# Performance work log

Hardware: AMD Instinct MI355X
Metric: run time of the kernel (lower is better)

## Reference

```python
import jax, jax.numpy as jnp
import numpy as np

H, DK = 8, 64
INNER = H * DK  # 512


def rel_shift(x):
    # Transformer-XL relative shift (NeMo style): pad left, reshape, drop first row.
    b, h, q, p = x.shape
    x = jnp.pad(x, ((0, 0), (0, 0), (0, 0), (1, 0)))
    x = x.reshape(b, h, p + 1, q)[:, :, 1:]
    return x.reshape(b, h, q, p)


def setup_inputs() -> dict:
    key = jax.random.key(0)
    ks = jax.random.split(key, 16)
    B, T, D = 8, 1024, 512
    s_d = 1.0 / np.sqrt(D)
    s_i = 1.0 / np.sqrt(INNER)
    return {
        "x": jax.random.normal(ks[0], (B, T, D), jnp.float32),
        "pos_emb": jax.random.normal(ks[1], (1, 2 * T - 1, INNER), jnp.float32),
        "w_qkv": jax.random.normal(ks[2], (D, 3 * INNER), jnp.float32) * s_d,
        "w_q": jax.random.normal(ks[3], (INNER, INNER), jnp.float32) * s_i,
        "b_q": jnp.zeros((INNER,), jnp.float32),
        "w_k": jax.random.normal(ks[4], (INNER, INNER), jnp.float32) * s_i,
        "b_k": jnp.zeros((INNER,), jnp.float32),
        "w_v": jax.random.normal(ks[5], (INNER, INNER), jnp.float32) * s_i,
        "b_v": jnp.zeros((INNER,), jnp.float32),
        "w_pos": jax.random.normal(ks[6], (INNER, INNER), jnp.float32) * s_i,
        "bias_u": jax.random.normal(ks[7], (H, DK), jnp.float32) * 0.02,
        "bias_v": jax.random.normal(ks[8], (H, DK), jnp.float32) * 0.02,
        "w_ao": jax.random.normal(ks[9], (INNER, INNER), jnp.float32) * s_i,
        "b_ao": jnp.zeros((INNER,), jnp.float32),
        "w_o": jax.random.normal(ks[10], (INNER, D), jnp.float32) * s_i,
        "b_o": jnp.zeros((D,), jnp.float32),
    }


def reference(x, pos_emb, w_qkv, w_q, b_q, w_k, b_k, w_v, b_v, w_pos,
              bias_u, bias_v, w_ao, b_ao, w_o, b_o):
    B, T, D = x.shape
    # wrapper qkv projection (no bias), then chunk
    q, k, v = jnp.split(x @ w_qkv, 3, axis=-1)
    # RelPositionMultiHeadAttention internal projections
    q = (q @ w_q + b_q).reshape(B, T, H, DK)                       # (b,t,h,d)
    k = (k @ w_k + b_k).reshape(B, T, H, DK).transpose(0, 2, 1, 3)  # (b,h,t,d)
    v = (v @ w_v + b_v).reshape(B, T, H, DK).transpose(0, 2, 1, 3)  # (b,h,t,d)
    p = (pos_emb @ w_pos).reshape(pos_emb.shape[0], -1, H, DK).transpose(0, 2, 1, 3)  # (1,h,2t-1,d)
    q_u = (q + bias_u).transpose(0, 2, 1, 3)  # (b,h,t,d)
    q_v = (q + bias_v).transpose(0, 2, 1, 3)
    matrix_ac = jnp.einsum('bhqd,bhkd->bhqk', q_u, k)      # (b,h,t,t)
    matrix_bd = jnp.einsum('bhqd,xhpd->bhqp', q_v, p)      # (b,h,t,2t-1)
    matrix_bd = rel_shift(matrix_bd)[..., :T]
    scores = (matrix_ac + matrix_bd) * (1.0 / np.sqrt(DK))
    attn = jax.nn.softmax(scores, axis=-1)  # mask=None, dropout inactive at eval
    out = jnp.einsum('bhqk,bhkd->bhqd', attn, v)
    out = out.transpose(0, 2, 1, 3).reshape(B, T, INNER)
    out = out @ w_ao + b_ao   # attention linear_out
    return out @ w_o + b_o    # wrapper to_out
```

## Files before the change

### kernel.cpp

```cpp
#include <hip/hip_runtime.h>
#include <hip/hip_bf16.h>
#include <math.h>

#define H_     8
#define DK_    64
#define INNER_ 512
#define B_     8
#define T_     1024
#define D_     512
#define PLEN_  2047
#define BT_    8192

typedef __attribute__((ext_vector_type(8))) short bf16x8;
typedef __attribute__((ext_vector_type(4))) float f32x4;
typedef __attribute__((ext_vector_type(4))) unsigned short u16x4;
typedef __attribute__((ext_vector_type(8))) unsigned short u16x8;

__device__ __forceinline__ unsigned short f2bf(float f) {
    unsigned u = __float_as_uint(f);
    u += 0x7fffu + ((u >> 16) & 1u);
    return (unsigned short)(u >> 16);
}
__device__ __forceinline__ float bf2f(unsigned short s) {
    return __uint_as_float(((unsigned)s) << 16);
}
__device__ __forceinline__ f32x4 mfma16(bf16x8 a, bf16x8 b, f32x4 c) {
    return __builtin_amdgcn_mfma_f32_16x16x32_bf16(a, b, c, 0, 0, 0);
}
__device__ __forceinline__ void gload16(const unsigned short* g, unsigned short* l) {
    __builtin_amdgcn_global_load_lds(
        (const __attribute__((address_space(1))) void*)g,
        (__attribute__((address_space(3))) void*)l,
        16, 0, 0);
}
#define BARRIER()  __builtin_amdgcn_s_barrier()
#define SCHEDBAR() __builtin_amdgcn_sched_barrier(0)
#define VMCNT(N)   asm volatile("s_waitcnt vmcnt(" #N ")" ::: "memory")

#define QSCALE 0.125f

struct SplitA {
    const float* s[4];
    unsigned short* h[4];
    unsigned short* l[4];
    long n[4];
};
__global__ __launch_bounds__(256) void split4(SplitA a)
{
    const int seg = blockIdx.y;
    long i4 = ((long)blockIdx.x * 256 + threadIdx.x) * 4;
    if (i4 >= a.n[seg]) return;
    f32x4 v = *(const f32x4*)(a.s[seg] + i4);
    u16x4 hh, ll;
    #pragma unroll
    for (int i = 0; i < 4; ++i) {
        unsigned short hb = f2bf(v[i]);
        hh[i] = hb;
        ll[i] = f2bf(v[i] - bf2f(hb));
    }
    *(u16x4*)(a.h[seg] + i4) = hh;
    *(u16x4*)(a.l[seg] + i4) = ll;
}

struct PrepW {
    const float* w[5];
    unsigned short* wh[5];
    unsigned short* wl[5];
};
__global__ __launch_bounds__(256) void prep_wb(PrepW p)
{
    const int z = blockIdx.z;
    const float* w = p.w[z];
    unsigned short* wh = p.wh[z];
    unsigned short* wl = p.wl[z];
    __shared__ float sW[32][36];
    const int t = threadIdx.x;
    const int n0 = blockIdx.x * 32, k0 = blockIdx.y * 32;
    {
        int kr = t >> 3, c4 = (t & 7) * 4;
        f32x4 v = *(const f32x4*)(w + (size_t)(k0 + kr) * 512 + n0 + c4);
        #pragma unroll
        for (int i = 0; i < 4; ++i) sW[kr][c4 + i] = v[i];
    }
    __syncthreads();
    {
        int nr = t >> 3, kc = (t & 7) * 4;
        u16x4 hv, lv;
        #pragma unroll
        for (int i = 0; i < 4; ++i) {
            float f = sW[kc + i][nr];
            unsigned short hb = f2bf(f);
            hv[i] = hb;
            lv[i] = f2bf(f - bf2f(hb));
        }
        *(u16x4*)(wh + (size_t)(n0 + nr) * 512 + k0 + kc) = hv;
        *(u16x4*)(wl + (size_t)(n0 + nr) * 512 + k0 + kc) = lv;
    }
}

__global__ __launch_bounds__(256) void misc_k(
    const float* __restrict__ b_ao, const float* __restrict__ w_o,
    const float* __restrict__ b_o, float* __restrict__ be,
    unsigned short* __restrict__ pb_base)
{
    if (blockIdx.x < 2) {
        int n = blockIdx.x * 256 + threadIdx.x;
        float s = b_o[n];
        for (int j = 0; j < 512; ++j) s += b_ao[j] * w_o[(size_t)j * 512 + n];
        be[n] = s;
    } else {
        ((unsigned int*)pb_base)[threadIdx.x] = 0u;
    }
}

template<int MF, bool ALO>
__device__ __forceinline__ void gemm_core(
    f32x4 (&acc)[MF][4],
    const unsigned short* __restrict__ Ah_g,
    const unsigned short* __restrict__ Al_g, int lda,
    const unsigned short* __restrict__ Wh_g,
    const unsigned short* __restrict__ Wl_g,
    int M, int row0, int col0,
    unsigned short* sAh, unsigned short* sAl,
    unsigned short* sWh, unsigned short* sWl)
{
    const int t = threadIdx.x;
    const int lane = t & 63, w = t >> 6;
    const int wm = w >> 1, wn = w & 1;
    const int ln15 = lane & 15, g4 = lane >> 4;
    const int ASZ = MF * 32 * 32;
    const int WSZ = 128 * 32;
    constexpr int NLD = (MF / 2) * (ALO ? 2 : 1) + 4;

    auto stage = [&](int kt, int buf) {
        #pragma unroll
        for (int l = 0; l < MF / 2; ++l) {
            int e = l * 256 + w * 64 + lane;
            int row = e >> 2, slot = e & 3;
            int ss = slot ^ (row & 3);
            int gr = row0 + row;
            if (gr > M - 1) gr = M - 1;
            size_t ga = (size_t)gr * lda + kt * 32 + ss * 8;
            gload16(Ah_g + ga, sAh + buf * ASZ + (l * 256 + w * 64) * 8);
            if constexpr (ALO)
                gload16(Al_g + ga, sAl + buf * ASZ + (l * 256 + w * 64) * 8);
        }
        #pragma unroll
        for (int l = 0; l < 2; ++l) {
            int e = l * 256 + w * 64 + lane;
            int row = e >> 2, slot = e & 3;
            int ss = slot ^ (row & 3);
            size_t gw = (size_t)(col0 + row) * 512 + kt * 32 + ss * 8;
            gload16(Wh_g + gw, sWh + buf * WSZ + (l * 256 + w * 64) * 8);
            gload16(Wl_g + gw, sWl + buf * WSZ + (l * 256 + w * 64) * 8);
        }
    };
    auto comp = [&](int buf) {
        bf16x8 fah[MF], fal[MF], fwh[4], fwl[4];
        #pragma unroll
        for (int i = 0; i < MF; ++i) {
            int ar = wm * (MF * 16) + i * 16 + ln15;
            int sa = (g4 ^ (ar & 3)) * 8;
            fah[i] = *(const bf16x8*)&sAh[buf * ASZ + ar * 32 + sa];
            if constexpr (ALO)
                fal[i] = *(const bf16x8*)&sAl[buf * ASZ + ar * 32 + sa];
        }
        #pragma unroll
        for (int j = 0; j < 4; ++j) {
            int wr = wn * 64 + j * 16 + ln15;
            int sw = (g4 ^ (wr & 3)) * 8;
            fwh[j] = *(const bf16x8*)&sWh[buf * WSZ + wr * 32 + sw];
            fwl[j] = *(const bf16x8*)&sWl[buf * WSZ + wr * 32 + sw];
        }
        __builtin_amdgcn_s_setprio(1);
        #pragma unroll
        for (int mi = 0; mi < MF; ++mi)
            #pragma unroll
            for (int ni = 0; ni < 4; ++ni) {
                acc[mi][ni] = mfma16(fah[mi], fwh[ni], acc[mi][ni]);
                acc[mi][ni] = mfma16(fah[mi], fwl[ni], acc[mi][ni]);
                if constexpr (ALO)
                    acc[mi][ni] = mfma16(fal[mi], fwh[ni], acc[mi][ni]);
            }
        __builtin_amdgcn_s_setprio(0);
    };

    stage(0, 0);
    for (int k2 = 0; k2 < 8; ++k2) {
        BARRIER();
        stage(2 * k2 + 1, 1);
        if constexpr (NLD == 6) { VMCNT(6); } else { VMCNT(8); }
        BARRIER(); SCHEDBAR();
        comp(0);
        BARRIER();
        if (k2 < 7) {
            stage(2 * k2 + 2, 0);
            if constexpr (NLD == 6) { VMCNT(6); } else { VMCNT(8); }
        } else {
            VMCNT(0);
        }
        BARRIER(); SCHEDBAR();
        comp(1);
    }
}

#define GEMM_LDS3(MF) \
    __shared__ __align__(16) unsigned short sAh[2][MF * 32 * 32]; \
    __shared__ __align__(16) unsigned short sAl[2][MF * 32 * 32]; \
    __shared__ __align__(16) unsigned short sWh[2][128 * 32];     \
    __shared__ __align__(16) unsigned short sWl[2][128 * 32];
#define GEMM_LDS2(MF) \
    __shared__ __align__(16) unsigned short sAh[2][MF * 32 * 32]; \
    __shared__ __align__(16) unsigned short sWh[2][128 * 32];     \
    __shared__ __align__(16) unsigned short sWl[2][128 * 32];

__global__ __launch_bounds__(256, 3) void gemm_qkv(
    const unsigned short* __restrict__ Ah_g,
    const unsigned short* __restrict__ Wh_g,
    const unsigned short* __restrict__ Wl_g,
    const float* __restrict__ b_q, const float* __restrict__ bu,
    const float* __restrict__ bv, const float* __restrict__ b_k,
    const float* __restrict__ b_v,
    unsigned short* __restrict__ qu, unsigned short* __restrict__ qv,
    unsigned short* __restrict__ kb, unsigned short* __restrict__ vt)
{
    GEMM_LDS2(4)
    f32x4 acc[4][4];
    #pragma unroll
    for (int i = 0; i < 4; ++i)
        #pragma unroll
        for (int j = 0; j < 4; ++j) acc[i][j] = (f32x4){0.f, 0.f, 0.f, 0.f};
    const int row0 = blockIdx.y * 128, col0 = blockIdx.x * 128;
    gemm_core<4, false>(acc, Ah_g, nullptr, 512, Wh_g, Wl_g, BT_, row0, col0,
                        &sAh[0][0], &sAh[0][0], &sWh[0][0], &sWl[0][0]);

    const int t = threadIdx.x;
    const int lane = t & 63, w = t >> 6;
    const int wm = w >> 1, wn = w & 1;
    const int ln15 = lane & 15, g4 = lane >> 4;
    const int grp = col0 >> 9;

    if (grp == 2) {
        #pragma unroll
        for (int mi = 0; mi < 4; ++mi) {
            int gr0 = row0 + wm * 64 + mi * 16 + g4 * 4;
            int bb = gr0 >> 10, t0 = gr0 & 1023;
            #pragma unroll
            for (int ni = 0; ni < 4; ++ni) {
                int gcl = (col0 & 511) + wn * 64 + ni * 16 + ln15;
                float bias = b_v[gcl];
                u16x4 vv;
                #pragma unroll
                for (int r4 = 0; r4 < 4; ++r4) vv[r4] = f2bf(acc[mi][ni][r4] + bias);
                *(u16x4*)(vt + ((size_t)(bb * 512 + gcl)) * 1024 + t0) = vv;
            }
        }
    } else {
        #pragma unroll
        for (int mi = 0; mi < 4; ++mi)
            #pragma unroll
            for (int r4 = 0; r4 < 4; ++r4) {
                int gr = row0 + wm * 64 + mi * 16 + g4 * 4 + r4;
                #pragma unroll
                for (int ni = 0; ni < 4; ++ni) {
                    int gcl = (col0 & 511) + wn * 64 + ni * 16 + ln15;
                    float a = acc[mi][ni][r4];
                    if (grp == 0) {
                        float base = a + b_q[gcl];
                        qu[(size_t)gr * 512 + gcl] = f2bf((base + bu[gcl]) * QSCALE);
                        qv[(size_t)gr * 512 + gcl] = f2bf((base + bv[gcl]) * QSCALE);
                    } else {
                        kb[(size_t)gr * 512 + gcl] = f2bf(a + b_k[gcl]);
                    }
                }
            }
    }
}

__global__ __launch_bounds__(256, 3) void gemm_pos(
    const unsigned short* __restrict__ Ah_g,
    const unsigned short* __restrict__ Wh_g,
    const unsigned short* __restrict__ Wl_g,
    unsigned short* __restrict__ pb0)
{
    GEMM_LDS2(4)
    f32x4 acc[4][4];
    #pragma unroll
    for (int i = 0; i < 4; ++i)
        #pragma unroll
        for (int j = 0; j < 4; ++j) acc[i][j] = (f32x4){0.f, 0.f, 0.f, 0.f};
    const int row0 = blockIdx.y * 128, col0 = blockIdx.x * 128;
    gemm_core<4, false>(acc, Ah_g, nullptr, 512, Wh_g, Wl_g, PLEN_, row0, col0,
                        &sAh[0][0], &sAh[0][0], &sWh[0][0], &sWl[0][0]);

    const int t = threadIdx.x;
    const int lane = t & 63, w = t >> 6;
    const int wm = w >> 1, wn = w & 1;
    const int ln15 = lane & 15, g4 = lane >> 4;
    #pragma unroll
    for (int mi = 0; mi < 4; ++mi)
        #pragma unroll
        for (int r4 = 0; r4 < 4; ++r4) {
            int gr = row0 + wm * 64 + mi * 16 + g4 * 4 + r4;
            if (gr >= PLEN_) continue;
            #pragma unroll
            for (int ni = 0; ni < 4; ++ni) {
                int gc = col0 + wn * 64 + ni * 16 + ln15;
                pb0[(size_t)gr * 512 + gc] = f2bf(acc[mi][ni][r4]);
            }
        }
}

struct WeffA {
    const unsigned short* ah[4];
    const unsigned short* al[4];
    int lda[4];
    const unsigned short* wh[4];
    const unsigned short* wl[4];
    float* c[4];
};
__global__ __launch_bounds__(256, 3) void gemm_weff(WeffA a)
{
    GEMM_LDS3(2)
    const int z = blockIdx.z;
    f32x4 acc[2][4];
    #pragma unroll
    for (int i = 0; i < 2; ++i)
        #pragma unroll
        for (int j = 0; j < 4; ++j) acc[i][j] = (f32x4){0.f, 0.f, 0.f, 0.f};
    const int row0 = blockIdx.y * 64, col0 = blockIdx.x * 128;
    gemm_core<2, true>(acc, a.ah[z], a.al[z], a.lda[z], a.wh[z], a.wl[z],
                       512, row0, col0,
                       &sAh[0][0], &sAl[0][0], &sWh[0][0], &sWl[0][0]);

    const int t = threadIdx.x;
    const int lane = t & 63, w = t >> 6;
    const int wm = w >> 1, wn = w & 1;
    const int ln15 = lane & 15, g4 = lane >> 4;
    float* C = a.c[z];
    #pragma unroll
    for (int mi = 0; mi < 2; ++mi)
        #pragma unroll
        for (int r4 = 0; r4 < 4; ++r4) {
            int gr = row0 + wm * 32 + mi * 16 + g4 * 4 + r4;
            #pragma unroll
            for (int ni = 0; ni < 4; ++ni) {
                int gc = col0 + wn * 64 + ni * 16 + ln15;
                C[(size_t)gr * 512 + gc] = acc[mi][ni][r4];
            }
        }
}

__global__ __launch_bounds__(256, 3) void gemm_out(
    const unsigned short* __restrict__ Ah_g,
    const unsigned short* __restrict__ Al_g,
    const unsigned short* __restrict__ Wh_g,
    const unsigned short* __restrict__ Wl_g,
    const float* __restrict__ beff, float* __restrict__ C)
{
    GEMM_LDS3(2)
    f32x4 acc[2][4];
    #pragma unroll
    for (int i = 0; i < 2; ++i)
        #pragma unroll
        for (int j = 0; j < 4; ++j) acc[i][j] = (f32x4){0.f, 0.f, 0.f, 0.f};
    const int row0 = blockIdx.y * 64, col0 = blockIdx.x * 128;
    gemm_core<2, true>(acc, Ah_g, Al_g, 512, Wh_g, Wl_g, BT_, row0, col0,
                       &sAh[0][0], &sAl[0][0], &sWh[0][0], &sWl[0][0]);

    const int t = threadIdx.x;
    const int lane = t & 63, w = t >> 6;
    const int wm = w >> 1, wn = w & 1;
    const int ln15 = lane & 15, g4 = lane >> 4;
    #pragma unroll
    for (int mi = 0; mi < 2; ++mi)
        #pragma unroll
        for (int r4 = 0; r4 < 4; ++r4) {
            int gr = row0 + wm * 32 + mi * 16 + g4 * 4 + r4;
            #pragma unroll
            for (int ni = 0; ni < 4; ++ni) {
                int gc = col0 + wn * 64 + ni * 16 + ln15;
                C[(size_t)gr * 512 + gc] = acc[mi][ni][r4] + beff[gc];
            }
        }
}

__global__ __launch_bounds__(256, 2) void attn_v9(
    const unsigned short* __restrict__ qu_g,
    const unsigned short* __restrict__ qv_g,
    const unsigned short* __restrict__ kb_g,
    const unsigned short* __restrict__ vt_g,
    const unsigned short* __restrict__ pb_g,
    unsigned short* __restrict__ atth,
    unsigned short* __restrict__ attl)
{
    __shared__ __align__(16) unsigned short sK[2][64 * 64];
    __shared__ __align__(16) unsigned short sP[2][64 * 64];
    __shared__ __align__(16) unsigned short sV[2][64 * 64];
    __shared__ __align__(16) unsigned short ringb[64][132];
    __shared__ __align__(16) unsigned short sProb[64][72];

    const int t = threadIdx.x;
    const int lane = t & 63, w = t >> 6;
    const int ln15 = lane & 15, g4 = lane >> 4;

    const int wg = blockIdx.x;
    const int idx = (wg & 7) * 128 + (wg >> 3);
    const int q0 = (idx & 15) * 64;
    const int bh = idx >> 4;
    const int h = bh & 7, b = bh >> 3;
    const size_t tok0 = (size_t)b * T_;
    const int hd = h * DK_;
    const int qq = w * 16 + ln15;

    auto stage_chunk = [&](int c, int buf) {
        #pragma unroll
        for (int l = 0; l < 2; ++l) {
            int e = l * 256 + w * 64 + lane;
            int row = e >> 3, slot = e & 7;
            int sl = slot ^ (row & 7);
            int lofs = buf * 4096 + (l * 256 + w * 64) * 8;
            gload16(kb_g + (tok0 + c * 64 + row) * INNER_ + hd + sl * 8, &sK[0][lofs]);
            gload16(vt_g + ((size_t)(b * H_ + h) * DK_ + row) * T_ + c * 64 + sl * 8, &sV[0][lofs]);
            long p = (long)(c * 64 - q0 + 1023 + row);
            gload16(pb_g + p * INNER_ + hd + sl * 8, &sP[0][lofs]);
        }
    };

    #pragma unroll
    for (int l = 0; l < 2; ++l) {
        int e = l * 256 + w * 64 + lane;
        int row = e >> 3, slot = e & 7;
        int sl = slot ^ (row & 7);
        size_t src = (tok0 + q0 + row) * INNER_ + hd + sl * 8;
        gload16(qu_g + src, &sK[0][(l * 256 + w * 64) * 8]);
        gload16(qv_g + src, &sP[0][(l * 256 + w * 64) * 8]);
    }
    __syncthreads();
    bf16x8 fqu[2], fqv[2];
    #pragma unroll
    for (int ki = 0; ki < 2; ++ki) {
        int sl = (ki * 4 + g4) ^ (qq & 7);
        fqu[ki] = *(const bf16x8*)&sK[0][qq * 64 + sl * 8];
        fqv[ki] = *(const bf16x8*)&sP[0][qq * 64 + sl * 8];
    }
    __syncthreads();

    #pragma unroll
    for (int l = 0; l < 2; ++l) {
        int e = l * 256 + w * 64 + lane;
        int row = e >> 3, slot = e & 7;
        int sl = slot ^ (row & 7);
        long p = (long)(959 - q0 + row);
        gload16(pb_g + p * INNER_ + hd + sl * 8, &sP[0][4096 + (l * 256 + w * 64) * 8]);
    }
    stage_chunk(0, 0);
    VMCNT(6);
    BARRIER(); SCHEDBAR();

    #pragma unroll
    for (int n = 0; n < 4; ++n) {
        f32x4 bdv = {0.f, 0.f, 0.f, 0.f};
        #pragma unroll
        for (int ki = 0; ki < 2; ++ki) {
            int prow = n * 16 + ln15;
            int sl = (ki * 4 + g4) ^ (prow & 7);
            bf16x8 pf = *(const bf16x8*)&sP[0][4096 + prow * 64 + sl * 8];
            bdv = mfma16(pf, fqv[ki], bdv);
        }
        #pragma unroll
        for (int r4 = 0; r4 < 4; ++r4)
            ringb[qq][(n * 16 + g4 * 4 + r4 + qq) & 127] = f2bf(bdv[r4]);
    }

    float m = -1e30f, den = 0.f;
    f32x4 o[4];
    #pragma unroll
    for (int i = 0; i < 4; ++i) o[i] = (f32x4){0.f, 0.f, 0.f, 0.f};

    auto compute_chunk = [&](int c, int buf) {
        const int bofs = buf * 4096;
        f32x4 sc[4], bd[4];
        #pragma unroll
        for (int n = 0; n < 4; ++n) {
            sc[n] = (f32x4){0.f, 0.f, 0.f, 0.f};
            bd[n] = (f32x4){0.f, 0.f, 0.f, 0.f};
        }
        __builtin_amdgcn_s_setprio(1);
        #pragma unroll
        for (int ki = 0; ki < 2; ++ki)
            #pragma unroll
            for (int n = 0; n < 4; ++n) {
                int krow = n * 16 + ln15;
                int sl = (ki * 4 + g4) ^ (krow & 7);
                bf16x8 kf = *(const bf16x8*)&sK[0][bofs + krow * 64 + sl * 8];
                sc[n] = mfma16(kf, fqu[ki], sc[n]);
                bf16x8 pf = *(const bf16x8*)&sP[0][bofs + krow * 64 + sl * 8];
                bd[n] = mfma16(pf, fqv[ki], bd[n]);
            }
        __builtin_amdgcn_s_setprio(0);

        const int pbase = (c & 1) ? 0 : 64;
        #pragma unroll
        for (int n = 0; n < 4; ++n)
            #pragma unroll
            for (int r4 = 0; r4 < 4; ++r4)
                ringb[qq][(pbase + n * 16 + g4 * 4 + r4 + qq) & 127] = f2bf(bd[n][r4]);

        float s[4][4];
        float mx = -1e30f;
        #pragma unroll
        for (int n = 0; n < 4; ++n) {
            const int st2 = (c * 64 + 64 + n * 16 + g4 * 4) & 127;
            u16x4 rv = *(const u16x4*)&ringb[qq][st2];
            #pragma unroll
            for (int r4 = 0; r4 < 4; ++r4) {
                float v = sc[n][r4] + bf2f(rv[r4]);
                s[n][r4] = v;
                mx = fmaxf(mx, v);
            }
        }
        mx = fmaxf(mx, __shfl_xor(mx, 16));
        mx = fmaxf(mx, __shfl_xor(mx, 32));
        float newm = fmaxf(m, mx);
        float scale = __expf(m - newm);
        m = newm;
        float ls = 0.f;
        #pragma unroll
        for (int n = 0; n < 4; ++n) {
            u16x4 pv4;
            #pragma unroll
            for (int r4 = 0; r4 < 4; ++r4) {
                float p = __expf(s[n][r4] - newm);
                ls += p;
                pv4[r4] = f2bf(p);
            }
            *(u16x4*)&sProb[qq][n * 16 + g4 * 4] = pv4;
        }
        ls += __shfl_xor(ls, 16);
        ls += __shfl_xor(ls, 32);
        den = den * scale + ls;
        #pragma unroll
        for (int n2 = 0; n2 < 4; ++n2) {
            o[n2][0] *= scale; o[n2][1] *= scale;
            o[n2][2] *= scale; o[n2][3] *= scale;
        }

        __builtin_amdgcn_s_setprio(1);
        #pragma unroll
        for (int ki = 0; ki < 2; ++ki) {
            bf16x8 pa = *(const bf16x8*)&sProb[qq][ki * 32 + g4 * 8];
            #pragma unroll
            for (int n2 = 0; n2 < 4; ++n2) {
                int drow = n2 * 16 + ln15;
                int sl = (ki * 4 + g4) ^ (drow & 7);
                bf16x8 vf = *(const bf16x8*)&sV[0][bofs + drow * 64 + sl * 8];
                o[n2] = mfma16(vf, pa, o[n2]);
            }
        }
        __builtin_amdgcn_s_setprio(0);
    };

    for (int c2 = 0; c2 < 8; ++c2) {
        const int c = 2 * c2;
        BARRIER();
        stage_chunk(c + 1, 1);
        VMCNT(6);
        BARRIER(); SCHEDBAR();
        compute_chunk(c, 0);

        BARRIER();
        if (c2 < 7) {
            stage_chunk(c + 2, 0);
            VMCNT(6);
        } else {
            VMCNT(0);
        }
        BARRIER(); SCHEDBAR();
        compute_chunk(c + 1, 1);
    }

    const float inv = 1.0f / den;
    #pragma unroll
    for (int n2 = 0; n2 < 4; ++n2) {
        u16x4 hv, lv;
        #pragma unroll
        for (int r4 = 0; r4 < 4; ++r4) {
            float val = o[n2][r4] * inv;
            unsigned short hb = f2bf(val);
            hv[r4] = hb;
            lv[r4] = f2bf(val - bf2f(hb));
        }
        size_t oidx = (tok0 + q0 + qq) * INNER_ + hd + n2 * 16 + g4 * 4;
        *(u16x4*)(atth + oidx) = hv;
        *(u16x4*)(attl + oidx) = lv;
    }
}

extern "C" void kernel_launch(void* const* d_in, const int* in_sizes, int n_in,
                              void* d_out, int out_size, void* d_ws, size_t ws_size,
                              hipStream_t stream)
{
    const float* x     = (const float*)d_in[0];
    const float* pos   = (const float*)d_in[1];
    const float* w_qkv = (const float*)d_in[2];
    const float* w_q   = (const float*)d_in[3];
    const float* b_q   = (const float*)d_in[4];
    const float* w_k   = (const float*)d_in[5];
    const float* b_k   = (const float*)d_in[6];
    const float* w_v   = (const float*)d_in[7];
    const float* b_v   = (const float*)d_in[8];
    const float* w_pos = (const float*)d_in[9];
    const float* bu    = (const float*)d_in[10];
    const float* bv    = (const float*)d_in[11];
    const float* w_ao  = (const float*)d_in[12];
    const float* b_ao  = (const float*)d_in[13];
    const float* w_o   = (const float*)d_in[14];
    const float* b_o   = (const float*)d_in[15];
    float* out = (float*)d_out;

    unsigned short* u = (unsigned short*)d_ws;
    const size_t SZ = (size_t)BT_ * INNER_;
    unsigned short* xh   = u;
    unsigned short* xl   = xh + SZ;
    unsigned short* qu   = xl + SZ;
    unsigned short* qv   = qu + SZ;
    unsigned short* kb   = qv + SZ;
    unsigned short* vt   = kb + SZ;
    unsigned short* atth = vt + SZ;
    unsigned short* attl = atth + SZ;
    unsigned short* pb_base = attl + SZ;
    unsigned short* pb0  = pb_base + 512;
    unsigned short* posh = pb_base + 1049600;
    unsigned short* posl = posh + 1049600;
    unsigned short* wqkvh = posl + 1049600;
    unsigned short* wqkvl = wqkvh + 786432;
    unsigned short* waoh  = wqkvl + 786432;
    unsigned short* waol  = waoh + 262144;
    unsigned short* w5    = waol + 262144;
    unsigned short* wq_h = w5;              unsigned short* wq_l = w5 + 262144;
    unsigned short* wk_h = w5 + 2*262144;   unsigned short* wk_l = w5 + 3*262144;
    unsigned short* wv_h = w5 + 4*262144;   unsigned short* wv_l = w5 + 5*262144;
    unsigned short* wo_h = w5 + 6*262144;   unsigned short* wo_l = w5 + 7*262144;
    unsigned short* wp_h = w5 + 8*262144;   unsigned short* wp_l = w5 + 9*262144;
    float* weffC = (float*)(w5 + 10*262144);
    unsigned short* wcat_h = (unsigned short*)(weffC + 4*262144);
    unsigned short* wcat_l = wcat_h + 786432;
    unsigned short* woe_h  = wcat_l + 786432;
    unsigned short* woe_l  = woe_h + 262144;
    float* beff = (float*)(woe_l + 262144);

    dim3 blk(256);

    SplitA sa;
    sa.s[0] = x;     sa.h[0] = xh;    sa.l[0] = xl;    sa.n[0] = (long)SZ;
    sa.s[1] = w_qkv; sa.h[1] = wqkvh; sa.l[1] = wqkvl; sa.n[1] = 786432L;
    sa.s[2] = w_ao;  sa.h[2] = waoh;  sa.l[2] = waol;  sa.n[2] = 262144L;
    sa.s[3] = pos;   sa.h[3] = posh;  sa.l[3] = posl;  sa.n[3] = (long)PLEN_ * 512;
    split4<<<dim3(4096, 4), blk, 0, stream>>>(sa);

    PrepW p5;
    p5.w[0] = w_q;   p5.wh[0] = wq_h; p5.wl[0] = wq_l;
    p5.w[1] = w_k;   p5.wh[1] = wk_h; p5.wl[1] = wk_l;
    p5.w[2] = w_v;   p5.wh[2] = wv_h; p5.wl[2] = wv_l;
    p5.w[3] = w_o;   p5.wh[3] = wo_h; p5.wl[3] = wo_l;
    p5.w[4] = w_pos; p5.wh[4] = wp_h; p5.wl[4] = wp_l;
    prep_wb<<<dim3(16, 16, 5), blk, 0, stream>>>(p5);

    WeffA wa;
    wa.ah[0] = wqkvh;        wa.al[0] = wqkvl;        wa.lda[0] = 1536;
    wa.ah[1] = wqkvh + 512;  wa.al[1] = wqkvl + 512;  wa.lda[1] = 1536;
    wa.ah[2] = wqkvh + 1024; wa.al[2] = wqkvl + 1024; wa.lda[2] = 1536;
    wa.ah[3] = waoh;         wa.al[3] = waol;         wa.lda[3] = 512;
    wa.wh[0] = wq_h; wa.wl[0] = wq_l;
    wa.wh[1] = wk_h; wa.wl[1] = wk_l;
    wa.wh[2] = wv_h; wa.wl[2] = wv_l;
    wa.wh[3] = wo_h; wa.wl[3] = wo_l;
    wa.c[0] = weffC;             wa.c[1] = weffC + 262144;
    wa.c[2] = weffC + 2*262144;  wa.c[3] = weffC + 3*262144;
    gemm_weff<<<dim3(4, 8, 4), blk, 0, stream>>>(wa);

    PrepW p4;
    p4.w[0] = weffC;            p4.wh[0] = wcat_h;            p4.wl[0] = wcat_l;
    p4.w[1] = weffC + 262144;   p4.wh[1] = wcat_h + 262144;   p4.wl[1] = wcat_l + 262144;
    p4.w[2] = weffC + 2*262144; p4.wh[2] = wcat_h + 2*262144; p4.wl[2] = wcat_l + 2*262144;
    p4.w[3] = weffC + 3*262144; p4.wh[3] = woe_h;             p4.wl[3] = woe_l;
    p4.w[4] = nullptr; p4.wh[4] = nullptr; p4.wl[4] = nullptr;
    prep_wb<<<dim3(16, 16, 4), blk, 0, stream>>>(p4);

    misc_k<<<3, blk, 0, stream>>>(b_ao, w_o, b_o, beff, pb_base);

    gemm_qkv<<<dim3(12, 64), blk, 0, stream>>>(xh, wcat_h, wcat_l,
        b_q, bu, bv, b_k, b_v, qu, qv, kb, vt);
    gemm_pos<<<dim3(4, 16), blk, 0, stream>>>(posh, wp_h, wp_l, pb0);

    attn_v9<<<1024, blk, 0, stream>>>(qu, qv, kb, vt, pb0, atth, attl);

    gemm_out<<<dim3(4, 128), blk, 0, stream>>>(atth, attl, woe_h, woe_l, beff, out);
}
```

Measured before the change: 195.5 us.

## Halve attention KV chunk size to raise occupancy and skip unused low splits

The attention kernel now processes 32-key chunks instead of 64. This halves the shared-memory staging buffers and probability tile, and lets launch bounds target three workgroups per CU instead of two. The pipeline becomes a simple double buffer over 32 iterations, and the relative-position ring buffer indexing is reworked to match. Separately, the split kernel skips writing low-part bf16 halves for x and pos_emb, which downstream code does not use. The cost is twice as many barriers and loop iterations, and shorter MFMA runs per barrier.

```diff
diff --git a/kernel.cpp b/kernel.cpp
--- a/kernel.cpp
+++ b/kernel.cpp
@@ -44,6 +44,7 @@
     unsigned short* h[4];
     unsigned short* l[4];
     long n[4];
+    int wantl[4];
 };
 __global__ __launch_bounds__(256) void split4(SplitA a)
 {
@@ -59,7 +60,7 @@
         ll[i] = f2bf(v[i] - bf2f(hb));
     }
     *(u16x4*)(a.h[seg] + i4) = hh;
-    *(u16x4*)(a.l[seg] + i4) = ll;
+    if (a.wantl[seg]) *(u16x4*)(a.l[seg] + i4) = ll;
 }
 
 struct PrepW {
@@ -385,7 +386,7 @@
         }
 }
 
-__global__ __launch_bounds__(256, 2) void attn_v9(
+__global__ __launch_bounds__(256, 3) void attn_v10(
     const unsigned short* __restrict__ qu_g,
     const unsigned short* __restrict__ qv_g,
     const unsigned short* __restrict__ kb_g,
@@ -394,11 +395,11 @@
     unsigned short* __restrict__ atth,
     unsigned short* __restrict__ attl)
 {
-    __shared__ __align__(16) unsigned short sK[2][64 * 64];
-    __shared__ __align__(16) unsigned short sP[2][64 * 64];
-    __shared__ __align__(16) unsigned short sV[2][64 * 64];
+    __shared__ __align__(16) unsigned short sK[2][2048];
+    __shared__ __align__(16) unsigned short sP[2][2048];
+    __shared__ __align__(16) unsigned short sV[2][2048];
     __shared__ __align__(16) unsigned short ringb[64][132];
-    __shared__ __align__(16) unsigned short sProb[64][72];
+    __shared__ __align__(16) unsigned short sProb[64][36];
 
     const int t = threadIdx.x;
     const int lane = t & 63, w = t >> 6;
@@ -414,64 +415,79 @@
     const int qq = w * 16 + ln15;
 
     auto stage_chunk = [&](int c, int buf) {
-        #pragma unroll
-        for (int l = 0; l < 2; ++l) {
-            int e = l * 256 + w * 64 + lane;
+        int e = w * 64 + lane;
+        {
             int row = e >> 3, slot = e & 7;
             int sl = slot ^ (row & 7);
-            int lofs = buf * 4096 + (l * 256 + w * 64) * 8;
-            gload16(kb_g + (tok0 + c * 64 + row) * INNER_ + hd + sl * 8, &sK[0][lofs]);
-            gload16(vt_g + ((size_t)(b * H_ + h) * DK_ + row) * T_ + c * 64 + sl * 8, &sV[0][lofs]);
-            long p = (long)(c * 64 - q0 + 1023 + row);
-            gload16(pb_g + p * INNER_ + hd + sl * 8, &sP[0][lofs]);
+            gload16(kb_g + (tok0 + c * 32 + row) * INNER_ + hd + sl * 8,
+                    &sK[buf][w * 512]);
+        }
+        {
+            int row = e >> 2, slot = e & 3;
+            int sl = slot ^ (row & 3);
+            gload16(vt_g + ((size_t)(b * H_ + h) * DK_ + row) * T_ + c * 32 + sl * 8,
+                    &sV[buf][w * 512]);
+        }
+        {
+            int row = e >> 3, slot = e & 7;
+            int sl = slot ^ (row & 7);
+            long p = (long)(c * 32 - q0 + 1023 + row);
+            gload16(pb_g + p * INNER_ + hd + sl * 8, &sP[buf][w * 512]);
         }
     };
 
+    const unsigned short* sKf = &sK[0][0];
+    const unsigned short* sPf = &sP[0][0];
     #pragma unroll
     for (int l = 0; l < 2; ++l) {
-        int e = l * 256 + w * 64 + lane;
+        int e = l * 256 + t;
         int row = e >> 3, slot = e & 7;
         int sl = slot ^ (row & 7);
         size_t src = (tok0 + q0 + row) * INNER_ + hd + sl * 8;
-        gload16(qu_g + src, &sK[0][(l * 256 + w * 64) * 8]);
-        gload16(qv_g + src, &sP[0][(l * 256 + w * 64) * 8]);
+        gload16(qu_g + src, &sK[l][w * 512]);
+        gload16(qv_g + src, &sP[l][w * 512]);
     }
     __syncthreads();
     bf16x8 fqu[2], fqv[2];
     #pragma unroll
     for (int ki = 0; ki < 2; ++ki) {
         int sl = (ki * 4 + g4) ^ (qq & 7);
-        fqu[ki] = *(const bf16x8*)&sK[0][qq * 64 + sl * 8];
-        fqv[ki] = *(const bf16x8*)&sP[0][qq * 64 + sl * 8];
+        fqu[ki] = *(const bf16x8*)&sKf[qq * 64 + sl * 8];
+        fqv[ki] = *(const bf16x8*)&sPf[qq * 64 + sl * 8];
     }
     __syncthreads();
 
     #pragma unroll
     for (int l = 0; l < 2; ++l) {
-        int e = l * 256 + w * 64 + lane;
+        int e = l * 256 + t;
         int row = e >> 3, slot = e & 7;
         int sl = slot ^ (row & 7);
         long p = (long)(959 - q0 + row);
-        gload16(pb_g + p * INNER_ + hd + sl * 8, &sP[0][4096 + (l * 256 + w * 64) * 8]);
-    }
+        gload16(pb_g + p * INNER_ + hd + sl * 8, &sP[l][w * 512]);
+    }
+    VMCNT(0);
+    BARRIER(); SCHEDBAR();
+
+    #pragma unroll
+    for (int hh2 = 0; hh2 < 2; ++hh2)
+        #pragma unroll
+        for (int n = 0; n < 2; ++n) {
+            f32x4 bdv = {0.f, 0.f, 0.f, 0.f};
+            #pragma unroll
+            for (int ki = 0; ki < 2; ++ki) {
+                int prow = hh2 * 32 + n * 16 + ln15;
+                int sl = (ki * 4 + g4) ^ (prow & 7);
+                bf16x8 pf = *(const bf16x8*)&sPf[prow * 64 + sl * 8];
+                bdv = mfma16(pf, fqv[ki], bdv);
+            }
+            #pragma unroll
+            for (int r4 = 0; r4 < 4; ++r4)
+                ringb[qq][(hh2 * 32 + n * 16 + g4 * 4 + r4 + qq + 64) & 127] =
+                    f2bf(bdv[r4]);
+        }
+    BARRIER();
+
     stage_chunk(0, 0);
-    VMCNT(6);
-    BARRIER(); SCHEDBAR();
-
-    #pragma unroll
-    for (int n = 0; n < 4; ++n) {
-        f32x4 bdv = {0.f, 0.f, 0.f, 0.f};
-        #pragma unroll
-        for (int ki = 0; ki < 2; ++ki) {
-            int prow = n * 16 + ln15;
-            int sl = (ki * 4 + g4) ^ (prow & 7);
-            bf16x8 pf = *(const bf16x8*)&sP[0][4096 + prow * 64 + sl * 8];
-            bdv = mfma16(pf, fqv[ki], bdv);
-        }
-        #pragma unroll
-        for (int r4 = 0; r4 < 4; ++r4)
-            ringb[qq][(n * 16 + g4 * 4 + r4 + qq) & 127] = f2bf(bdv[r4]);
-    }
 
     float m = -1e30f, den = 0.f;
     f32x4 o[4];
@@ -479,10 +495,9 @@
     for (int i = 0; i < 4; ++i) o[i] = (f32x4){0.f, 0.f, 0.f, 0.f};
 
     auto compute_chunk = [&](int c, int buf) {
-        const int bofs = buf * 4096;
-        f32x4 sc[4], bd[4];
-        #pragma unroll
-        for (int n = 0; n < 4; ++n) {
+        f32x4 sc[2], bd[2];
+        #pragma unroll
+        for (int n = 0; n < 2; ++n) {
             sc[n] = (f32x4){0.f, 0.f, 0.f, 0.f};
             bd[n] = (f32x4){0.f, 0.f, 0.f, 0.f};
         }
@@ -490,28 +505,28 @@
         #pragma unroll
         for (int ki = 0; ki < 2; ++ki)
             #pragma unroll
-            for (int n = 0; n < 4; ++n) {
+            for (int n = 0; n < 2; ++n) {
                 int krow = n * 16 + ln15;
                 int sl = (ki * 4 + g4) ^ (krow & 7);
-                bf16x8 kf = *(const bf16x8*)&sK[0][bofs + krow * 64 + sl * 8];
+                bf16x8 kf = *(const bf16x8*)&sK[buf][krow * 64 + sl * 8];
                 sc[n] = mfma16(kf, fqu[ki], sc[n]);
-                bf16x8 pf = *(const bf16x8*)&sP[0][bofs + krow * 64 + sl * 8];
+                bf16x8 pf = *(const bf16x8*)&sP[buf][krow * 64 + sl * 8];
                 bd[n] = mfma16(pf, fqv[ki], bd[n]);
             }
         __builtin_amdgcn_s_setprio(0);
 
-        const int pbase = (c & 1) ? 0 : 64;
-        #pragma unroll
-        for (int n = 0; n < 4; ++n)
+        #pragma unroll
+        for (int n = 0; n < 2; ++n)
             #pragma unroll
             for (int r4 = 0; r4 < 4; ++r4)
-                ringb[qq][(pbase + n * 16 + g4 * 4 + r4 + qq) & 127] = f2bf(bd[n][r4]);
-
-        float s[4][4];
+                ringb[qq][(c * 32 + n * 16 + g4 * 4 + r4 + qq) & 127] =
+                    f2bf(bd[n][r4]);
+
+        float s[2][4];
         float mx = -1e30f;
         #pragma unroll
-        for (int n = 0; n < 4; ++n) {
-            const int st2 = (c * 64 + 64 + n * 16 + g4 * 4) & 127;
+        for (int n = 0; n < 2; ++n) {
+            const int st2 = (c * 32 + n * 16 + g4 * 4) & 127;
             u16x4 rv = *(const u16x4*)&ringb[qq][st2];
             #pragma unroll
             for (int r4 = 0; r4 < 4; ++r4) {
@@ -527,7 +542,7 @@
         m = newm;
         float ls = 0.f;
         #pragma unroll
-        for (int n = 0; n < 4; ++n) {
+        for (int n = 0; n < 2; ++n) {
             u16x4 pv4;
             #pragma unroll
             for (int r4 = 0; r4 < 4; ++r4) {
@@ -547,37 +562,27 @@
         }
 
         __builtin_amdgcn_s_setprio(1);
-        #pragma unroll
-        for (int ki = 0; ki < 2; ++ki) {
-            bf16x8 pa = *(const bf16x8*)&sProb[qq][ki * 32 + g4 * 8];
-            #pragma unroll
-            for (int n2 = 0; n2 < 4; ++n2) {
-                int drow = n2 * 16 + ln15;
-                int sl = (ki * 4 + g4) ^ (drow & 7);
-                bf16x8 vf = *(const bf16x8*)&sV[0][bofs + drow * 64 + sl * 8];
-                o[n2] = mfma16(vf, pa, o[n2]);
-            }
+        bf16x8 pa = *(const bf16x8*)&sProb[qq][g4 * 8];
+        #pragma unroll
+        for (int n2 = 0; n2 < 4; ++n2) {
+            int drow = n2 * 16 + ln15;
+            int sl4 = g4 ^ (drow & 3);
+            bf16x8 vf = *(const bf16x8*)&sV[buf][drow * 32 + sl4 * 8];
+            o[n2] = mfma16(vf, pa, o[n2]);
         }
         __builtin_amdgcn_s_setprio(0);
     };
 
-    for (int c2 = 0; c2 < 8; ++c2) {
-        const int c = 2 * c2;
+    for (int c = 0; c < 32; ++c) {
         BARRIER();
-        stage_chunk(c + 1, 1);
-        VMCNT(6);
-        BARRIER(); SCHEDBAR();
-        compute_chunk(c, 0);
-
-        BARRIER();
-        if (c2 < 7) {
-            stage_chunk(c + 2, 0);
-            VMCNT(6);
+        if (c < 31) {
+            stage_chunk(c + 1, (c + 1) & 1);
+            VMCNT(3);
         } else {
             VMCNT(0);
         }
         BARRIER(); SCHEDBAR();
-        compute_chunk(c + 1, 1);
+        compute_chunk(c, c & 1);
     }
 
     const float inv = 1.0f / den;
@@ -653,10 +658,10 @@
     dim3 blk(256);
 
     SplitA sa;
-    sa.s[0] = x;     sa.h[0] = xh;    sa.l[0] = xl;    sa.n[0] = (long)SZ;
-    sa.s[1] = w_qkv; sa.h[1] = wqkvh; sa.l[1] = wqkvl; sa.n[1] = 786432L;
-    sa.s[2] = w_ao;  sa.h[2] = waoh;  sa.l[2] = waol;  sa.n[2] = 262144L;
-    sa.s[3] = pos;   sa.h[3] = posh;  sa.l[3] = posl;  sa.n[3] = (long)PLEN_ * 512;
+    sa.s[0] = x;     sa.h[0] = xh;    sa.l[0] = xl;    sa.n[0] = (long)SZ;          sa.wantl[0] = 0;
+    sa.s[1] = w_qkv; sa.h[1] = wqkvh; sa.l[1] = wqkvl; sa.n[1] = 786432L;           sa.wantl[1] = 1;
+    sa.s[2] = w_ao;  sa.h[2] = waoh;  sa.l[2] = waol;  sa.n[2] = 262144L;           sa.wantl[2] = 1;
+    sa.s[3] = pos;   sa.h[3] = posh;  sa.l[3] = posl;  sa.n[3] = (long)PLEN_ * 512; sa.wantl[3] = 0;
     split4<<<dim3(4096, 4), blk, 0, stream>>>(sa);
 
     PrepW p5;
@@ -694,7 +699,7 @@
         b_q, bu, bv, b_k, b_v, qu, qv, kb, vt);
     gemm_pos<<<dim3(4, 16), blk, 0, stream>>>(posh, wp_h, wp_l, pb0);
 
-    attn_v9<<<1024, blk, 0, stream>>>(qu, qv, kb, vt, pb0, atth, attl);
+    attn_v10<<<1024, blk, 0, stream>>>(qu, qv, kb, vt, pb0, atth, attl);
 
     gemm_out<<<dim3(4, 128), blk, 0, stream>>>(atth, attl, woe_h, woe_l, beff, out);
 }
```

Result: slower. 211.7 us (+8.3%).

## Fuse pos GEMM into QKV GEMM launch, skip unused low splits, simplify attention sync

Applied to the files above, without the earlier changes.

Merges the positional projection GEMM into the QKV GEMM grid as an extra column of blocks, removing one launch and letting the two GEMMs run concurrently. The split kernel no longer writes low-part bf16 halves for x and pos_emb, since those are never read. In the attention kernel, the hand-tuned partial vmcnt waits and raw barriers are replaced with plain __syncthreads, which waits for all outstanding loads each step and may lose the prefetch/compute overlap.

```diff
diff --git a/kernel.cpp b/kernel.cpp
--- a/kernel.cpp
+++ b/kernel.cpp
@@ -44,6 +44,7 @@
     unsigned short* h[4];
     unsigned short* l[4];
     long n[4];
+    int wantl[4];
 };
 __global__ __launch_bounds__(256) void split4(SplitA a)
 {
@@ -59,7 +60,7 @@
         ll[i] = f2bf(v[i] - bf2f(hb));
     }
     *(u16x4*)(a.h[seg] + i4) = hh;
-    *(u16x4*)(a.l[seg] + i4) = ll;
+    if (a.wantl[seg]) *(u16x4*)(a.l[seg] + i4) = ll;
 }
 
 struct PrepW {
@@ -214,15 +215,19 @@
     __shared__ __align__(16) unsigned short sWh[2][128 * 32];     \
     __shared__ __align__(16) unsigned short sWl[2][128 * 32];
 
-__global__ __launch_bounds__(256, 3) void gemm_qkv(
+__global__ __launch_bounds__(256, 3) void gemm_qkvp(
     const unsigned short* __restrict__ Ah_g,
     const unsigned short* __restrict__ Wh_g,
     const unsigned short* __restrict__ Wl_g,
+    const unsigned short* __restrict__ posh,
+    const unsigned short* __restrict__ wp_h,
+    const unsigned short* __restrict__ wp_l,
     const float* __restrict__ b_q, const float* __restrict__ bu,
     const float* __restrict__ bv, const float* __restrict__ b_k,
     const float* __restrict__ b_v,
     unsigned short* __restrict__ qu, unsigned short* __restrict__ qv,
-    unsigned short* __restrict__ kb, unsigned short* __restrict__ vt)
+    unsigned short* __restrict__ kb, unsigned short* __restrict__ vt,
+    unsigned short* __restrict__ pb0)
 {
     GEMM_LDS2(4)
     f32x4 acc[4][4];
@@ -230,16 +235,43 @@
     for (int i = 0; i < 4; ++i)
         #pragma unroll
         for (int j = 0; j < 4; ++j) acc[i][j] = (f32x4){0.f, 0.f, 0.f, 0.f};
-    const int row0 = blockIdx.y * 128, col0 = blockIdx.x * 128;
-    gemm_core<4, false>(acc, Ah_g, nullptr, 512, Wh_g, Wl_g, BT_, row0, col0,
+
+    const int bx = blockIdx.x, by = blockIdx.y;
+    const bool isPos = (bx == 12);
+    int row0, col0, M;
+    const unsigned short *Ag, *Whg, *Wlg;
+    if (isPos) {
+        row0 = (by >> 2) * 128; col0 = (by & 3) * 128;
+        Ag = posh; Whg = wp_h; Wlg = wp_l; M = PLEN_;
+    } else {
+        row0 = by * 128; col0 = bx * 128;
+        Ag = Ah_g; Whg = Wh_g; Wlg = Wl_g; M = BT_;
+    }
+    gemm_core<4, false>(acc, Ag, nullptr, 512, Whg, Wlg, M, row0, col0,
                         &sAh[0][0], &sAh[0][0], &sWh[0][0], &sWl[0][0]);
 
     const int t = threadIdx.x;
     const int lane = t & 63, w = t >> 6;
     const int wm = w >> 1, wn = w & 1;
     const int ln15 = lane & 15, g4 = lane >> 4;
+
+    if (isPos) {
+        #pragma unroll
+        for (int mi = 0; mi < 4; ++mi)
+            #pragma unroll
+            for (int r4 = 0; r4 < 4; ++r4) {
+                int gr = row0 + wm * 64 + mi * 16 + g4 * 4 + r4;
+                if (gr >= PLEN_) continue;
+                #pragma unroll
+                for (int ni = 0; ni < 4; ++ni) {
+                    int gc = col0 + wn * 64 + ni * 16 + ln15;
+                    pb0[(size_t)gr * 512 + gc] = f2bf(acc[mi][ni][r4]);
+                }
+            }
+        return;
+    }
+
     const int grp = col0 >> 9;
-
     if (grp == 2) {
         #pragma unroll
         for (int mi = 0; mi < 4; ++mi) {
@@ -277,40 +309,6 @@
     }
 }
 
-__global__ __launch_bounds__(256, 3) void gemm_pos(
-    const unsigned short* __restrict__ Ah_g,
-    const unsigned short* __restrict__ Wh_g,
-    const unsigned short* __restrict__ Wl_g,
-    unsigned short* __restrict__ pb0)
-{
-    GEMM_LDS2(4)
-    f32x4 acc[4][4];
-    #pragma unroll
-    for (int i = 0; i < 4; ++i)
-        #pragma unroll
-        for (int j = 0; j < 4; ++j) acc[i][j] = (f32x4){0.f, 0.f, 0.f, 0.f};
-    const int row0 = blockIdx.y * 128, col0 = blockIdx.x * 128;
-    gemm_core<4, false>(acc, Ah_g, nullptr, 512, Wh_g, Wl_g, PLEN_, row0, col0,
-                        &sAh[0][0], &sAh[0][0], &sWh[0][0], &sWl[0][0]);
-
-    const int t = threadIdx.x;
-    const int lane = t & 63, w = t >> 6;
-    const int wm = w >> 1, wn = w & 1;
-    const int ln15 = lane & 15, g4 = lane >> 4;
-    #pragma unroll
-    for (int mi = 0; mi < 4; ++mi)
-        #pragma unroll
-        for (int r4 = 0; r4 < 4; ++r4) {
-            int gr = row0 + wm * 64 + mi * 16 + g4 * 4 + r4;
-            if (gr >= PLEN_) continue;
-            #pragma unroll
-            for (int ni = 0; ni < 4; ++ni) {
-                int gc = col0 + wn * 64 + ni * 16 + ln15;
-                pb0[(size_t)gr * 512 + gc] = f2bf(acc[mi][ni][r4]);
-            }
-        }
-}
-
 struct WeffA {
     const unsigned short* ah[4];
     const unsigned short* al[4];
@@ -385,7 +383,7 @@
         }
 }
 
-__global__ __launch_bounds__(256, 2) void attn_v9(
+__global__ __launch_bounds__(256, 2) void attn_v12(
     const unsigned short* __restrict__ qu_g,
     const unsigned short* __restrict__ qv_g,
     const unsigned short* __restrict__ kb_g,
@@ -455,8 +453,7 @@
         gload16(pb_g + p * INNER_ + hd + sl * 8, &sP[0][4096 + (l * 256 + w * 64) * 8]);
     }
     stage_chunk(0, 0);
-    VMCNT(6);
-    BARRIER(); SCHEDBAR();
+    __syncthreads();
 
     #pragma unroll
     for (int n = 0; n < 4; ++n) {
@@ -472,6 +469,7 @@
         for (int r4 = 0; r4 < 4; ++r4)
             ringb[qq][(n * 16 + g4 * 4 + r4 + qq) & 127] = f2bf(bdv[r4]);
     }
+    __syncthreads();
 
     float m = -1e30f, den = 0.f;
     f32x4 o[4];
@@ -562,22 +560,13 @@
     };
 
     for (int c2 = 0; c2 < 8; ++c2) {
-        const int c = 2 * c2;
-        BARRIER();
+        int c = c2 * 2;
         stage_chunk(c + 1, 1);
-        VMCNT(6);
-        BARRIER(); SCHEDBAR();
         compute_chunk(c, 0);
-
-        BARRIER();
-        if (c2 < 7) {
-            stage_chunk(c + 2, 0);
-            VMCNT(6);
-        } else {
-            VMCNT(0);
-        }
-        BARRIER(); SCHEDBAR();
+        __syncthreads();
+        if (c2 < 7) stage_chunk(c + 2, 0);
         compute_chunk(c + 1, 1);
+        __syncthreads();
     }
 
     const float inv = 1.0f / den;
@@ -653,10 +642,10 @@
     dim3 blk(256);
 
     SplitA sa;
-    sa.s[0] = x;     sa.h[0] = xh;    sa.l[0] = xl;    sa.n[0] = (long)SZ;
-    sa.s[1] = w_qkv; sa.h[1] = wqkvh; sa.l[1] = wqkvl; sa.n[1] = 786432L;
-    sa.s[2] = w_ao;  sa.h[2] = waoh;  sa.l[2] = waol;  sa.n[2] = 262144L;
-    sa.s[3] = pos;   sa.h[3] = posh;  sa.l[3] = posl;  sa.n[3] = (long)PLEN_ * 512;
+    sa.s[0] = x;     sa.h[0] = xh;    sa.l[0] = xl;    sa.n[0] = (long)SZ;          sa.wantl[0] = 0;
+    sa.s[1] = w_qkv; sa.h[1] = wqkvh; sa.l[1] = wqkvl; sa.n[1] = 786432L;           sa.wantl[1] = 1;
+    sa.s[2] = w_ao;  sa.h[2] = waoh;  sa.l[2] = waol;  sa.n[2] = 262144L;           sa.wantl[2] = 1;
+    sa.s[3] = pos;   sa.h[3] = posh;  sa.l[3] = posl;  sa.n[3] = (long)PLEN_ * 512; sa.wantl[3] = 0;
     split4<<<dim3(4096, 4), blk, 0, stream>>>(sa);
 
     PrepW p5;
@@ -690,11 +679,11 @@
 
     misc_k<<<3, blk, 0, stream>>>(b_ao, w_o, b_o, beff, pb_base);
 
-    gemm_qkv<<<dim3(12, 64), blk, 0, stream>>>(xh, wcat_h, wcat_l,
-        b_q, bu, bv, b_k, b_v, qu, qv, kb, vt);
-    gemm_pos<<<dim3(4, 16), blk, 0, stream>>>(posh, wp_h, wp_l, pb0);
-
-    attn_v9<<<1024, blk, 0, stream>>>(qu, qv, kb, vt, pb0, atth, attl);
+    gemm_qkvp<<<dim3(13, 64), blk, 0, stream>>>(xh, wcat_h, wcat_l,
+        posh, wp_h, wp_l,
+        b_q, bu, bv, b_k, b_v, qu, qv, kb, vt, pb0);
+
+    attn_v12<<<1024, blk, 0, stream>>>(qu, qv, kb, vt, pb0, atth, attl);
 
     gemm_out<<<dim3(4, 128), blk, 0, stream>>>(atth, attl, woe_h, woe_l, beff, out);
 }
```

Result: faster. 188.3 us (-3.7%).
